# Kernel optimization log

Hardware: AMD Instinct MI355X
Metric: run time of the kernel (lower is better)

Reference implementation:

```python
import jax, jax.numpy as jnp
import numpy as np

B, S, D, A = 16, 4096, 2048, 2048

def setup_inputs() -> dict:
    key = jax.random.key(0)
    k1, k2, k3, k4 = jax.random.split(key, 4)
    encode_state = jax.random.normal(k1, (B, S, D), dtype=jnp.float32)
    hid_state = jax.random.normal(k2, (B, D), dtype=jnp.float32)
    W = jax.random.normal(k3, (A, D), dtype=jnp.float32) * (1.0 / np.sqrt(D))
    b = jax.random.normal(k4, (A,), dtype=jnp.float32) * 0.01
    return {"encode_state": encode_state, "hid_state": hid_state, "W": W, "b": b}

def reference(encode_state, hid_state, W, b):
    # project both encoder states and decoder hidden state: y = x @ W.T + b
    enc_proj = jnp.einsum('bsd,ad->bsa', encode_state, W) + b   # [B,S,A]
    hid_proj = jnp.einsum('bd,ad->ba', hid_state, W) + b        # [B,A]
    scores = jnp.einsum('bsa,ba->bs', enc_proj, hid_proj)       # [B,S]
    probs = jax.nn.softmax(scores, axis=1)                      # softmax over seq dim
    context_vector = jnp.einsum('bs,bsd->bd', probs, encode_state)  # [B,D]
    return (scores, context_vector)
```

## Files before the change

### kernel.cpp

```cpp
#include <hip/hip_runtime.h>
#include <hip/hip_bf16.h>
#include <cstddef>

#define BB 16
#define SS 4096
#define DD 2048
#define AA 2048
#define NR 16
#define CH 256
#define ACH 64

__device__ inline unsigned int pk_bf16(float a, float b) {
  __hip_bfloat162 h2 = __float22bfloat162_rn(make_float2(a, b));
  return *reinterpret_cast<unsigned int*>(&h2);
}

__global__ __launch_bounds__(256) void hp_kernel(
    const float* __restrict__ hid, const float* __restrict__ W,
    const float* __restrict__ bias, float* __restrict__ hp) {
  int gw   = (blockIdx.x * 256 + threadIdx.x) >> 6;
  int lane = threadIdx.x & 63;
  int a = gw;
  const float4* Wr = reinterpret_cast<const float4*>(W + (size_t)a * DD);
  float acc[BB];
#pragma unroll
  for (int b = 0; b < BB; ++b) acc[b] = 0.f;
#pragma unroll
  for (int k = 0; k < 8; ++k) {
    float4 w4 = Wr[lane + 64 * k];
#pragma unroll
    for (int b = 0; b < BB; ++b) {
      float4 h4 = reinterpret_cast<const float4*>(hid + b * DD)[lane + 64 * k];
      acc[b] += w4.x * h4.x + w4.y * h4.y + w4.z * h4.z + w4.w * h4.w;
    }
  }
  float bi = bias[a];
#pragma unroll
  for (int b = 0; b < BB; ++b) {
    float s = acc[b];
#pragma unroll
    for (int off = 32; off; off >>= 1) s += __shfl_xor(s, off, 64);
    if (lane == 0) hp[b * AA + a] = s + bi;
  }
}

__global__ __launch_bounds__(256) void vpart_kernel(
    const float* __restrict__ hp, const float* __restrict__ W,
    float* __restrict__ vpart) {
  int t  = threadIdx.x;
  int ac = blockIdx.x & 63;
  int dc = blockIdx.x >> 6;
  int d0 = dc * 1024 + 4 * t;
  float4 acc[BB];
#pragma unroll
  for (int b = 0; b < BB; ++b) acc[b] = make_float4(0.f, 0.f, 0.f, 0.f);
  int abase = ac * 32;
  for (int i = 0; i < 32; ++i) {
    int a = abase + i;
    float4 w4 = *reinterpret_cast<const float4*>(W + (size_t)a * DD + d0);
#pragma unroll
    for (int b = 0; b < BB; ++b) {
      float h = hp[b * AA + a];
      acc[b].x += h * w4.x; acc[b].y += h * w4.y;
      acc[b].z += h * w4.z; acc[b].w += h * w4.w;
    }
  }
#pragma unroll
  for (int b = 0; b < BB; ++b)
    *reinterpret_cast<float4*>(vpart + (size_t)(ac * BB + b) * DD + d0) = acc[b];
}

__global__ __launch_bounds__(256) void finalize_kernel(
    const float* __restrict__ vpart, const float* __restrict__ hp,
    const float* __restrict__ bias, float* __restrict__ v,
    float* __restrict__ cvec) {
  if (blockIdx.x < 128) {
    int i = blockIdx.x * 256 + threadIdx.x;
    float s = 0.f;
#pragma unroll
    for (int c = 0; c < ACH; ++c) s += vpart[(size_t)c * (BB * DD) + i];
    v[i] = s;
  } else {
    int b = blockIdx.x - 128;
    int t = threadIdx.x;
    float s = 0.f;
    for (int i = t; i < AA; i += 256) s += bias[i] * hp[b * AA + i];
#pragma unroll
    for (int off = 32; off; off >>= 1) s += __shfl_xor(s, off, 64);
    __shared__ float red[4];
    if ((t & 63) == 0) red[t >> 6] = s;
    __syncthreads();
    if (t == 0) cvec[b] = red[0] + red[1] + red[2] + red[3];
  }
}

__global__ __launch_bounds__(256) void fused_kernel(
    const float* __restrict__ enc, const float* __restrict__ v,
    const float* __restrict__ cvec, float* __restrict__ scores,
    float* __restrict__ mpart, float* __restrict__ lpart,
    unsigned int* __restrict__ ctxpart ) {
  int gw   = blockIdx.x * 4 + (threadIdx.x >> 6);
  int lane = threadIdx.x & 63;
  int b  = gw >> 8;
  int ch = gw & (CH - 1);
  const float4* vp = reinterpret_cast<const float4*>(v + (size_t)b * DD);
  float cb = cvec[b];
  float4 acc[8];
#pragma unroll
  for (int k = 0; k < 8; ++k) acc[k] = make_float4(0.f, 0.f, 0.f, 0.f);
  float m_s = -1e30f;
  float l = 0.f, myscore = 0.f;
  const float4* rowp = reinterpret_cast<const float4*>(
      enc + (size_t)(b * SS + ch * NR) * DD);

#pragma unroll
  for (int r = 0; r < NR; ++r) {
    float4 e[8];
#pragma unroll
    for (int k = 0; k < 8; ++k) e[k] = rowp[(size_t)r * 512 + lane + 64 * k];
    float dot = 0.f;
#pragma unroll
    for (int k = 0; k < 8; ++k) {
      float4 vv = vp[lane + 64 * k];
      dot += e[k].x * vv.x + e[k].y * vv.y + e[k].z * vv.z + e[k].w * vv.w;
    }
#pragma unroll
    for (int off = 32; off; off >>= 1) dot += __shfl_xor(dot, off, 64);
    float score = dot + cb;
    if (lane == r) myscore = score;
    if (score > m_s + 40.f) {
      float rs = __expf(m_s - score);
      l *= rs;
#pragma unroll
      for (int k = 0; k < 8; ++k) {
        acc[k].x *= rs; acc[k].y *= rs; acc[k].z *= rs; acc[k].w *= rs;
      }
      m_s = score;
    }
    float p = __expf(score - m_s);
    l += p;
#pragma unroll
    for (int k = 0; k < 8; ++k) {
      acc[k].x += p * e[k].x;
      acc[k].y += p * e[k].y;
      acc[k].z += p * e[k].z;
      acc[k].w += p * e[k].w;
    }
  }

  if (lane < NR) scores[b * SS + ch * NR + lane] = myscore;
  if (lane == 0) { mpart[gw] = m_s; lpart[gw] = l; }
  uint2* cp = reinterpret_cast<uint2*>(ctxpart) + (size_t)gw * 512;
#pragma unroll
  for (int k = 0; k < 8; ++k) {
    uint2 u;
    u.x = pk_bf16(acc[k].x, acc[k].y);
    u.y = pk_bf16(acc[k].z, acc[k].w);
    cp[lane + 64 * k] = u;
  }
}

__global__ __launch_bounds__(256) void epilogue_kernel(
    const float* __restrict__ mpart, const float* __restrict__ lpart,
    const unsigned int* __restrict__ ctxpart, float* __restrict__ ctx) {
  int b  = blockIdx.x >> 3;
  int ds = blockIdx.x & 7;
  int t  = threadIdx.x;
  __shared__ float wsm[CH];
  __shared__ float redm[4], redl[4];
  float mt = mpart[b * CH + t];
  float lt = lpart[b * CH + t];
  float M = mt;
#pragma unroll
  for (int off = 32; off; off >>= 1) M = fmaxf(M, __shfl_xor(M, off, 64));
  if ((t & 63) == 0) redm[t >> 6] = M;
  __syncthreads();
  M = fmaxf(fmaxf(redm[0], redm[1]), fmaxf(redm[2], redm[3]));
  float w  = __expf(mt - M);
  float lw = lt * w;
#pragma unroll
  for (int off = 32; off; off >>= 1) lw += __shfl_xor(lw, off, 64);
  if ((t & 63) == 0) redl[t >> 6] = lw;
  __syncthreads();
  float L = redl[0] + redl[1] + redl[2] + redl[3];
  wsm[t] = w / L;
  __syncthreads();
  int du = ds * 128 + (t >> 1);
  bool hi = (t & 1);
  float acc = 0.f;
  const unsigned int* base = ctxpart + (size_t)(b * CH) * (DD / 2) + du;
  for (int c = 0; c < CH; ++c) {
    unsigned int u = base[(size_t)c * (DD / 2)];
    float e = __uint_as_float(hi ? (u & 0xffff0000u) : (u << 16));
    acc += wsm[c] * e;
  }
  ctx[b * DD + ds * 256 + t] = acc;
}

extern "C" void kernel_launch(void* const* d_in, const int* in_sizes, int n_in,
                              void* d_out, int out_size, void* d_ws, size_t ws_size,
                              hipStream_t stream) {
  const float* enc  = (const float*)d_in[0];
  const float* hid  = (const float*)d_in[1];
  const float* W    = (const float*)d_in[2];
  const float* bias = (const float*)d_in[3];

  float* out_scores = (float*)d_out;
  float* out_ctx    = (float*)d_out + BB * SS;

  float* ws    = (float*)d_ws;
  float* hp    = ws;
  float* vpart = hp + BB * AA;
  float* v     = vpart + ACH * BB * DD;
  float* cvec  = v + BB * DD;
  float* mpart = cvec + BB;
  float* lpart = mpart + BB * CH;
  unsigned int* ctxp = (unsigned int*)(lpart + BB * CH);

  hipLaunchKernelGGL(hp_kernel,       dim3(512),  dim3(256), 0, stream, hid, W, bias, hp);
  hipLaunchKernelGGL(vpart_kernel,    dim3(128),  dim3(256), 0, stream, hp, W, vpart);
  hipLaunchKernelGGL(finalize_kernel, dim3(144),  dim3(256), 0, stream, vpart, hp, bias, v, cvec);
  hipLaunchKernelGGL(fused_kernel,    dim3(1024), dim3(256), 0, stream,
                     enc, v, cvec, out_scores, mpart, lpart, ctxp);
  hipLaunchKernelGGL(epilogue_kernel, dim3(128),  dim3(256), 0, stream,
                     mpart, lpart, ctxp, out_ctx);
}
```

Before: 198.5 us.

## Stage v in LDS and double-buffer encoder row loads in fused kernel

The fused attention kernel now copies each batch's projected vector v into shared memory once per block and reads it from LDS instead of global memory. The row loop is rewritten with two register buffers so the next encoder row is prefetched while the current row is reduced and accumulated. The aim is to hide global load latency on the streaming encoder read. In exchange, register pressure roughly doubles for the row data, the launch bound of 256 is dropped, and the last iteration issues a redundant reload of the final row.

```diff
diff --git a/kernel.cpp b/kernel.cpp
--- a/kernel.cpp
+++ b/kernel.cpp
@@ -94,16 +94,25 @@
   }
 }
 
-__global__ __launch_bounds__(256) void fused_kernel(
+__global__ void fused_kernel(
     const float* __restrict__ enc, const float* __restrict__ v,
     const float* __restrict__ cvec, float* __restrict__ scores,
     float* __restrict__ mpart, float* __restrict__ lpart,
     unsigned int* __restrict__ ctxpart ) {
-  int gw   = blockIdx.x * 4 + (threadIdx.x >> 6);
-  int lane = threadIdx.x & 63;
+  __shared__ float vsh[DD];
+  int tid  = threadIdx.x;
+  int gw   = blockIdx.x * 4 + (tid >> 6);
+  int lane = tid & 63;
   int b  = gw >> 8;
   int ch = gw & (CH - 1);
-  const float4* vp = reinterpret_cast<const float4*>(v + (size_t)b * DD);
+  {
+    const float4* vp  = reinterpret_cast<const float4*>(v + (size_t)b * DD);
+    float4*       vs4 = reinterpret_cast<float4*>(vsh);
+    vs4[tid]       = vp[tid];
+    vs4[tid + 256] = vp[tid + 256];
+  }
+  __syncthreads();
+  const float4* vs4 = reinterpret_cast<const float4*>(vsh);
   float cb = cvec[b];
   float4 acc[8];
 #pragma unroll
@@ -112,41 +121,53 @@
   float l = 0.f, myscore = 0.f;
   const float4* rowp = reinterpret_cast<const float4*>(
       enc + (size_t)(b * SS + ch * NR) * DD);
-
-#pragma unroll
-  for (int r = 0; r < NR; ++r) {
-    float4 e[8];
-#pragma unroll
-    for (int k = 0; k < 8; ++k) e[k] = rowp[(size_t)r * 512 + lane + 64 * k];
-    float dot = 0.f;
-#pragma unroll
-    for (int k = 0; k < 8; ++k) {
-      float4 vv = vp[lane + 64 * k];
-      dot += e[k].x * vv.x + e[k].y * vv.y + e[k].z * vv.z + e[k].w * vv.w;
-    }
-#pragma unroll
-    for (int off = 32; off; off >>= 1) dot += __shfl_xor(dot, off, 64);
-    float score = dot + cb;
-    if (lane == r) myscore = score;
-    if (score > m_s + 40.f) {
-      float rs = __expf(m_s - score);
-      l *= rs;
-#pragma unroll
-      for (int k = 0; k < 8; ++k) {
-        acc[k].x *= rs; acc[k].y *= rs; acc[k].z *= rs; acc[k].w *= rs;
-      }
-      m_s = score;
-    }
-    float p = __expf(score - m_s);
-    l += p;
-#pragma unroll
-    for (int k = 0; k < 8; ++k) {
-      acc[k].x += p * e[k].x;
-      acc[k].y += p * e[k].y;
-      acc[k].z += p * e[k].z;
-      acc[k].w += p * e[k].w;
-    }
-  }
+  float4 eA[8], eB[8];
+#pragma unroll
+  for (int k = 0; k < 8; ++k) eA[k] = rowp[lane + 64 * k];
+
+#define STEP(CUR, NXT, R)                                                     \
+  {                                                                           \
+    int rn = ((R) + 1 < NR) ? (R) + 1 : (R);                                  \
+    _Pragma("unroll")                                                         \
+    for (int k = 0; k < 8; ++k)                                               \
+      NXT[k] = rowp[(size_t)rn * 512 + lane + 64 * k];                        \
+    float dot = 0.f;                                                          \
+    _Pragma("unroll")                                                         \
+    for (int k = 0; k < 8; ++k) {                                             \
+      float4 vv = vs4[lane + 64 * k];                                         \
+      dot += CUR[k].x * vv.x + CUR[k].y * vv.y + CUR[k].z * vv.z +            \
+             CUR[k].w * vv.w;                                                 \
+    }                                                                         \
+    _Pragma("unroll")                                                         \
+    for (int off = 32; off; off >>= 1) dot += __shfl_xor(dot, off, 64);       \
+    float score = dot + cb;                                                   \
+    if (lane == (R)) myscore = score;                                         \
+    if (score > m_s + 40.f) {                                                 \
+      float rs = __expf(m_s - score);                                         \
+      l *= rs;                                                                \
+      _Pragma("unroll")                                                       \
+      for (int k = 0; k < 8; ++k) {                                           \
+        acc[k].x *= rs; acc[k].y *= rs; acc[k].z *= rs; acc[k].w *= rs;       \
+      }                                                                       \
+      m_s = score;                                                            \
+    }                                                                         \
+    float p = __expf(score - m_s);                                            \
+    l += p;                                                                   \
+    _Pragma("unroll")                                                         \
+    for (int k = 0; k < 8; ++k) {                                             \
+      acc[k].x += p * CUR[k].x;                                               \
+      acc[k].y += p * CUR[k].y;                                               \
+      acc[k].z += p * CUR[k].z;                                               \
+      acc[k].w += p * CUR[k].w;                                               \
+    }                                                                         \
+  }
+
+#pragma unroll
+  for (int rr = 0; rr < NR; rr += 2) {
+    STEP(eA, eB, rr)
+    STEP(eB, eA, rr + 1)
+  }
+#undef STEP
 
   if (lane < NR) scores[b * SS + ch * NR + lane] = myscore;
   if (lane == 0) { mpart[gw] = m_s; lpart[gw] = l; }
```

Measured after the change: 216.5 us. +9.1%, slower.
